# Kernel tuning notes

Hardware: AMD Instinct MI355X
Metric: run time of the kernel (lower is better)

Reference implementation:

```python
import jax, jax.numpy as jnp
import numpy as np

N, LQ, DM = 8, 2500, 256
NH, NL, NP, NZ = 8, 4, 8, 4
DH = DM // NH
SPATIAL = np.array([[64, 176], [32, 88], [16, 44], [8, 22]], dtype=np.int32)
LEN_IN = int((SPATIAL[:, 0] * SPATIAL[:, 1]).sum())


def setup_inputs() -> dict:
    key = jax.random.key(0)
    ks = jax.random.split(key, 10)
    query = jax.random.normal(ks[0], (N, LQ, DM), dtype=jnp.float32)
    query_pos = jax.random.normal(ks[1], (N, LQ, DM), dtype=jnp.float32)
    reference_points = jax.random.uniform(ks[2], (N, LQ, NZ, 2), dtype=jnp.float32)
    input_flatten = jax.random.normal(ks[3], (N, LEN_IN, DM), dtype=jnp.float32)
    input_spatial_shapes = jnp.asarray(SPATIAL)
    lsi = np.concatenate([[0], np.cumsum(SPATIAL[:, 0] * SPATIAL[:, 1])[:-1]]).astype(np.int32)
    input_level_start_index = jnp.asarray(lsi)
    # learned params (Linear: y = x @ W + b, W is (in, out))
    Wv = jax.random.normal(ks[4], (DM, DM), dtype=jnp.float32) * (1.0 / np.sqrt(DM))
    bv = jnp.zeros((DM,), dtype=jnp.float32)
    Wo = jax.random.normal(ks[5], (DM, NH * NL * NP * 2), dtype=jnp.float32) * 0.02
    bo = jax.random.normal(ks[6], (NH * NL * NP * 2,), dtype=jnp.float32) * 1.0
    Wa = jax.random.normal(ks[7], (DM, NH * NL * NP), dtype=jnp.float32) * 0.02
    ba = jnp.zeros((NH * NL * NP,), dtype=jnp.float32)
    return {"query": query, "query_pos": query_pos, "reference_points": reference_points,
            "input_flatten": input_flatten, "input_spatial_shapes": input_spatial_shapes,
            "input_level_start_index": input_level_start_index,
            "Wv": Wv, "bv": bv, "Wo": Wo, "bo": bo, "Wa": Wa, "ba": ba}


def _sample_level(v, h, w, loc):
    """Bilinear sample (grid_sample, align_corners=False, zero padding).
    v:   (N, h*w, NH, DH) level feature map
    loc: (N, Lq, NH, P, 2) normalized locations in [0,1] (x, y)
    returns (N, NH, Lq, P, DH)
    """
    n, hw, nh, dh = v.shape
    lq, p = loc.shape[1], loc.shape[3]
    x = loc[..., 0] * w - 0.5
    y = loc[..., 1] * h - 0.5
    x0f = jnp.floor(x)
    y0f = jnp.floor(y)
    wx = x - x0f
    wy = y - y0f
    x0 = x0f.astype(jnp.int32)
    y0 = y0f.astype(jnp.int32)
    vt = v.transpose(0, 2, 1, 3).reshape(n * nh, hw, dh)

    def gather(xi, yi, wgt):
        valid = ((xi >= 0) & (xi < w) & (yi >= 0) & (yi < h)).astype(v.dtype)
        idx = jnp.clip(yi, 0, h - 1) * w + jnp.clip(xi, 0, w - 1)  # (N,Lq,NH,P)
        idx = idx.transpose(0, 2, 1, 3).reshape(n * nh, lq * p)
        g = jnp.take_along_axis(vt, idx[:, :, None], axis=1)  # (N*NH, Lq*P, DH)
        wv = (wgt * valid).transpose(0, 2, 1, 3).reshape(n * nh, lq * p)
        return g * wv[:, :, None]

    out = (gather(x0, y0, (1 - wx) * (1 - wy))
           + gather(x0 + 1, y0, wx * (1 - wy))
           + gather(x0, y0 + 1, (1 - wx) * wy)
           + gather(x0 + 1, y0 + 1, wx * wy))
    return out.reshape(n, nh, lq, p, dh)


def _forward(query, query_pos, reference_points, input_flatten, spatial, Wv, bv, Wo, bo, Wa, ba):
    n, lq, _ = query.shape
    len_in = input_flatten.shape[1]
    # projections
    value = (input_flatten @ Wv + bv).reshape(n, len_in, NH, DH)
    off = (query @ Wo + bo).reshape(n, lq, NH, NL, NP, 2)
    aw = jax.nn.softmax((query @ Wa + ba).reshape(n, lq, NH, NL * NP), axis=-1)
    aw = aw.reshape(n, lq, NH, NL, NP)
    # normalize offsets by (W_l, H_l), add to Z-anchor reference points
    norm = jnp.asarray(np.stack([spatial[:, 1], spatial[:, 0]], -1), dtype=query.dtype)  # (NL,2)
    off = off / norm[None, None, None, :, None, :]
    off = off.reshape(n, lq, NH, NL, NP // NZ, NZ, 2)
    ref = reference_points[:, :, None, None, None, :, :]  # (N,Lq,1,1,1,NZ,2)
    loc = (ref + off).reshape(n, lq, NH, NL, NP, 2)
    # multi-scale deformable sampling + weighted reduction
    out = jnp.zeros((n, lq, NH, DH), dtype=query.dtype)
    start = 0
    for lvl in range(NL):
        h, w = int(spatial[lvl, 0]), int(spatial[lvl, 1])
        v_l = value[:, start:start + h * w]
        start += h * w
        samp = _sample_level(v_l, h, w, loc[:, :, :, lvl])  # (N,NH,Lq,NP,DH)
        out = out + jnp.einsum('nhqpd,nqhp->nqhd', samp, aw[:, :, :, lvl])
    return out.reshape(n, lq, DM)


def reference(query, query_pos, reference_points, input_flatten, input_spatial_shapes,
              input_level_start_index, Wv, bv, Wo, bo, Wa, ba):
    spatial = np.asarray(jax.device_get(input_spatial_shapes))
    return _forward(query, query_pos, reference_points, input_flatten, spatial,
                    Wv, bv, Wo, bo, Wa, ba)
```

## Files before the change

kernel.cpp:

```cpp
#include <hip/hip_runtime.h>
#include <hip/hip_fp16.h>

#define N_BATCH 8
#define LQ_     2500
#define DM_     256
#define NH_     8
#define NL_     4
#define NP_     8
#define DH_     32
#define LEN_IN_ 14960
#define KDIM    256

#define MV_   119680
#define MQ_   20000
#define NBMV  935
#define NBMQ  157
#define NVB   1872
#define NCB   960

__constant__ int c_w[4]     = {176, 88, 44, 22};
__constant__ int c_h[4]     = {64, 32, 16, 8};
__constant__ int c_start[4] = {0, 11264, 14080, 14784};

using bf16x8 = __attribute__((ext_vector_type(8))) short;
using f32x4  = __attribute__((ext_vector_type(4))) float;

#define GLDS16(g, l)                                                         \
    __builtin_amdgcn_global_load_lds(                                        \
        (const __attribute__((address_space(1))) void*)(g),                  \
        (__attribute__((address_space(3))) void*)(l), 16, 0, 0)

static __device__ inline float fdot2_u(unsigned int p, unsigned int w, float c) {
    float r;
    asm("v_dot2_f32_f16 %0, %1, %2, %3" : "=v"(r) : "v"(p), "v"(w), "v"(c));
    return r;
}

static __device__ inline void split_bf16(float v, unsigned short& hi, unsigned short& lo) {
    unsigned int u = __float_as_uint(v);
    hi = (unsigned short)(u >> 16);
    float hif = __uint_as_float(u & 0xFFFF0000u);
    float l = v - hif;
    lo = (unsigned short)(__float_as_uint(l) >> 16);
}

static __device__ inline unsigned short f2bf_rne(float v) {
    unsigned int u = __float_as_uint(v);
    u += 0x7FFFu + ((u >> 16) & 1u);
    return (unsigned short)(u >> 16);
}

static __device__ inline unsigned short f2h_rne(float v) {
    _Float16 h = (_Float16)v;
    return __builtin_bit_cast(unsigned short, h);
}

__global__ __launch_bounds__(256) void conv_weights(
    const float* __restrict__ Wv, const float* __restrict__ Wo,
    const float* __restrict__ Wa, const float* __restrict__ bo,
    const float* __restrict__ ba,
    unsigned short* __restrict__ Wv_hi, unsigned short* __restrict__ Wv_lo,
    unsigned short* __restrict__ Wc_hi, unsigned short* __restrict__ Wc_lo,
    float* __restrict__ bcomb)
{
    int id = blockIdx.x * 256 + threadIdx.x;
    if (id < 256 * 256) {
        int n = id >> 8, k = id & 255;
        unsigned short h, l;
        split_bf16(Wv[k * 256 + n], h, l);
        Wv_hi[id] = h; Wv_lo[id] = l;
    } else {
        int id2 = id - 65536;
        if (id2 < 768 * 256) {
            int n = id2 >> 8, k = id2 & 255;
            float v = (n < 512) ? Wo[k * 512 + n] : Wa[k * 256 + (n - 512)];
            unsigned short h, l;
            split_bf16(v, h, l);
            Wc_hi[id2] = h; Wc_lo[id2] = l;
        }
    }
    if (id < 768) bcomb[id] = (id < 512) ? bo[id] : ba[id - 512];
}

__global__ __launch_bounds__(512, 4) void gemm2(
    const float* __restrict__ Av,
    const float* __restrict__ Aq,
    const unsigned short* __restrict__ Wvh, const unsigned short* __restrict__ Wvl,
    const unsigned short* __restrict__ Wch, const unsigned short* __restrict__ Wcl,
    const float* __restrict__ bv, const float* __restrict__ bc,
    float* __restrict__ Cq,
    unsigned short* __restrict__ Cv)
{
    __shared__ __align__(16) unsigned short As [4096];
    __shared__ __align__(16) unsigned short Bhs[4096];
    __shared__ __align__(16) unsigned short Bls[4096];

    const int tid = threadIdx.x;
    const int bid = blockIdx.x;
    const bool is_comb = (bid >= NVB);

    const float* A;
    const unsigned short *Bth, *Btl;
    const float* bias;
    int by, bx, M, N;
    if (is_comb) {
        int cid = bid - NVB;
        int xcd = cid & 7, j = cid >> 3;
        by = xcd + 8 * (j / 6); bx = j % 6;
        if (by >= NBMQ) return;
        A = Aq; Bth = Wch; Btl = Wcl; bias = bc;
        M = MQ_; N = 768;
    } else {
        int xcd = bid & 7, j = bid >> 3;
        by = xcd + 8 * (j >> 1); bx = j & 1;
        if (by >= NBMV) return;
        A = Av; Bth = Wvh; Btl = Wvl; bias = bv;
        M = MV_; N = 256;
    }

    const int row0 = by << 7, col0 = bx << 7;
    const int lane = tid & 63, wave = tid >> 6;
    const int wrow = (wave & 1) << 6, wcol = (wave >> 1) << 5;
    const int r16  = lane & 15, quad = lane >> 4;

    const int srow = tid >> 2, skq = tid & 3;
    const int arow = min(row0 + srow, M - 1);
    const float* gA = A + (size_t)arow * KDIM + skq * 8;
    const unsigned short* gBh = Bth + (size_t)(col0 + srow) * KDIM + skq * 8;
    const unsigned short* gBl = Btl + (size_t)(col0 + srow) * KDIM + skq * 8;
    unsigned short* lBh = &Bhs[wave << 9];
    unsigned short* lBl = &Bls[wave << 9];
    const int aoff = srow * 32 + skq * 8;

    float4 pa[2][2];
#pragma unroll
    for (int s = 0; s < 2; ++s) {
        pa[s][0] = *(const float4*)(gA + s * 32);
        pa[s][1] = *(const float4*)(gA + s * 32 + 4);
    }

    f32x4 acc[4][2];
#pragma unroll
    for (int i = 0; i < 4; ++i)
#pragma unroll
        for (int j = 0; j < 2; ++j) acc[i][j] = (f32x4){0.f, 0.f, 0.f, 0.f};

#pragma unroll
    for (int kt = 0; kt < 8; ++kt) {
        const int cur = kt & 1;

        GLDS16(gBh + kt * 32, lBh);
        GLDS16(gBl + kt * 32, lBl);
        {
            bf16x8 hv;
            hv[0] = (short)f2bf_rne(pa[cur][0].x); hv[1] = (short)f2bf_rne(pa[cur][0].y);
            hv[2] = (short)f2bf_rne(pa[cur][0].z); hv[3] = (short)f2bf_rne(pa[cur][0].w);
            hv[4] = (short)f2bf_rne(pa[cur][1].x); hv[5] = (short)f2bf_rne(pa[cur][1].y);
            hv[6] = (short)f2bf_rne(pa[cur][1].z); hv[7] = (short)f2bf_rne(pa[cur][1].w);
            *(bf16x8*)&As[aoff] = hv;
        }
        __syncthreads();

        if (kt < 6) {
            pa[cur][0] = *(const float4*)(gA + (kt + 2) * 32);
            pa[cur][1] = *(const float4*)(gA + (kt + 2) * 32 + 4);
        }

        bf16x8 fbh[2], fbl[2], fa[4];
#pragma unroll
        for (int tn = 0; tn < 2; ++tn) {
            int n = wcol + tn * 16 + r16;
            fbh[tn] = *(const bf16x8*)&Bhs[n * 32 + (quad << 3)];
            fbl[tn] = *(const bf16x8*)&Bls[n * 32 + (quad << 3)];
        }
#pragma unroll
        for (int tm = 0; tm < 4; ++tm)
            fa[tm] = *(const bf16x8*)&As[(wrow + tm * 16 + r16) * 32 + (quad << 3)];
#pragma unroll
        for (int tm = 0; tm < 4; ++tm)
#pragma unroll
            for (int tn = 0; tn < 2; ++tn) {
                acc[tm][tn] = __builtin_amdgcn_mfma_f32_16x16x32_bf16(fa[tm], fbl[tn], acc[tm][tn], 0, 0, 0);
                acc[tm][tn] = __builtin_amdgcn_mfma_f32_16x16x32_bf16(fa[tm], fbh[tn], acc[tm][tn], 0, 0, 0);
            }
        __syncthreads();
    }

    float bvs[2];
#pragma unroll
    for (int tn = 0; tn < 2; ++tn) bvs[tn] = bias[col0 + wcol + tn * 16 + r16];
#pragma unroll
    for (int tm = 0; tm < 4; ++tm) {
#pragma unroll
        for (int i = 0; i < 4; ++i) {
            int row = row0 + wrow + tm * 16 + (quad << 2) + i;
            if (row < M) {
                if (is_comb) {
                    float* crow = Cq + (size_t)row * N + col0 + wcol + r16;
#pragma unroll
                    for (int tn = 0; tn < 2; ++tn)
                        crow[tn * 16] = acc[tm][tn][i] + bvs[tn];
                } else {
                    int n   = row / LEN_IN_;
                    int pix = row - n * LEN_IN_;
#pragma unroll
                    for (int tn = 0; tn < 2; ++tn) {
                        int col = col0 + wcol + tn * 16 + r16;
                        int h = col >> 5, dh = col & 31;
                        size_t addr = ((size_t)(n * NH_ + h) * LEN_IN_ + pix) * DH_ + dh;
                        Cv[addr] = f2h_rne(acc[tm][tn][i] + bvs[tn]);
                    }
                }
            }
        }
    }
}

__global__ __launch_bounds__(256, 4) void ms_sample(
    const unsigned short* __restrict__ value,
    const float* __restrict__ comb,
    const float* __restrict__ ref_pts,
    float* __restrict__ out)
{
    __shared__ uint4 s_desc[64][33];

    const int b     = blockIdx.x;
    const int xcd   = b & 7;
    const int j     = b >> 3;
    const int slice = (j / 40) * 8 + xcd;
    const int chunk = j % 40;
    const int n     = slice >> 3, h = slice & 7;
    const int q0    = chunk * 64;
    const int tid   = threadIdx.x;

    {
        int ql = tid >> 2, l = tid & 3;
        int q  = q0 + ql;
        if (q < LQ_) {
            int nq = n * LQ_ + q;
            const float* row = comb + (size_t)nq * 768;

            float4 L0 = *(const float4*)&row[512 + h * 32 + l * 8];
            float4 L1 = *(const float4*)&row[512 + h * 32 + l * 8 + 4];
            float lg[8] = {L0.x, L0.y, L0.z, L0.w, L1.x, L1.y, L1.z, L1.w};
            float m = lg[0];
#pragma unroll
            for (int i = 1; i < 8; ++i) m = fmaxf(m, lg[i]);
            m = fmaxf(m, __shfl_xor(m, 1));
            m = fmaxf(m, __shfl_xor(m, 2));
            float e[8], s = 0.f;
#pragma unroll
            for (int i = 0; i < 8; ++i) { e[i] = __expf(lg[i] - m); s += e[i]; }
            s += __shfl_xor(s, 1);
            s += __shfl_xor(s, 2);
            float inv = 1.f / s;

            float4 R0 = *(const float4*)&ref_pts[(size_t)nq * 8];
            float4 R1 = *(const float4*)&ref_pts[(size_t)nq * 8 + 4];
            float rx[4] = {R0.x, R0.z, R1.x, R1.z};
            float ry[4] = {R0.y, R0.w, R1.y, R1.w};

            float off[16];
#pragma unroll
            for (int i = 0; i < 4; ++i)
                *(float4*)&off[i * 4] = *(const float4*)&row[h * 64 + l * 16 + i * 4];

            float wl = (float)c_w[l], hl = (float)c_h[l];
            int wli = c_w[l], hli = c_h[l], st = c_start[l];
#pragma unroll
            for (int p = 0; p < 8; ++p) {
                int z = p & 3;
                float a = e[p] * inv;
                float x = rx[z] * wl + off[p * 2 + 0] - 0.5f;
                float y = ry[z] * hl + off[p * 2 + 1] - 0.5f;
                float x0f = floorf(x), y0f = floorf(y);
                int   x0 = (int)x0f,  y0 = (int)y0f;
                float wx = x - x0f,   wy = y - y0f;
                unsigned short ix[4];
                float wt[4];
#pragma unroll
                for (int jj = 0; jj < 4; ++jj) {
                    int xi = x0 + (jj & 1);
                    int yi = y0 + (jj >> 1);
                    float w = ((jj & 1) ? wx : 1.f - wx) * ((jj >> 1) ? wy : 1.f - wy);
                    bool valid = (xi >= 0) && (xi < wli) && (yi >= 0) && (yi < hli);
                    int xc = min(max(xi, 0), wli - 1);
                    int yc = min(max(yi, 0), hli - 1);
                    ix[jj] = (unsigned short)(yc * wli + xc);
                    wt[jj] = valid ? a * w : 0.f;
                }
                uint4 d;
                d.x = (unsigned int)(st + ix[0]) | ((unsigned int)(st + ix[1]) << 16);
                d.y = (unsigned int)(st + ix[2]) | ((unsigned int)(st + ix[3]) << 16);
                __half2 h01 = __floats2half2_rn(wt[0], wt[1]);
                __half2 h23 = __floats2half2_rn(wt[2], wt[3]);
                d.z = *(unsigned int*)&h01;
                d.w = *(unsigned int*)&h23;
                s_desc[ql][l * 8 + p] = d;
            }
        }
    }
    __syncthreads();

    int ql = tid >> 2, dhg = tid & 3;
    int q  = q0 + ql;
    if (q >= LQ_) return;
    int nq = n * LQ_ + q;
    const unsigned short* vb = value
        + ((size_t)(n * NH_ + h) * LEN_IN_) * DH_ + dhg * 8;

    float acc[8];
#pragma unroll
    for (int i = 0; i < 8; ++i) acc[i] = 0.f;

#pragma unroll 4
    for (int s = 0; s < 32; ++s) {
        uint4 d = s_desc[ql][s];
        int i0 = d.x & 0xFFFF, i1 = d.x >> 16;
        int i2 = d.y & 0xFFFF, i3 = d.y >> 16;
        uint4 v0 = *(const uint4*)(vb + i0 * DH_);
        uint4 v1 = *(const uint4*)(vb + i1 * DH_);
        uint4 v2 = *(const uint4*)(vb + i2 * DH_);
        uint4 v3 = *(const uint4*)(vb + i3 * DH_);
        acc[0] = fdot2_u(__builtin_amdgcn_perm(v1.x, v0.x, 0x05040100u), d.z, acc[0]);
        acc[1] = fdot2_u(__builtin_amdgcn_perm(v1.x, v0.x, 0x07060302u), d.z, acc[1]);
        acc[2] = fdot2_u(__builtin_amdgcn_perm(v1.y, v0.y, 0x05040100u), d.z, acc[2]);
        acc[3] = fdot2_u(__builtin_amdgcn_perm(v1.y, v0.y, 0x07060302u), d.z, acc[3]);
        acc[4] = fdot2_u(__builtin_amdgcn_perm(v1.z, v0.z, 0x05040100u), d.z, acc[4]);
        acc[5] = fdot2_u(__builtin_amdgcn_perm(v1.z, v0.z, 0x07060302u), d.z, acc[5]);
        acc[6] = fdot2_u(__builtin_amdgcn_perm(v1.w, v0.w, 0x05040100u), d.z, acc[6]);
        acc[7] = fdot2_u(__builtin_amdgcn_perm(v1.w, v0.w, 0x07060302u), d.z, acc[7]);
        acc[0] = fdot2_u(__builtin_amdgcn_perm(v3.x, v2.x, 0x05040100u), d.w, acc[0]);
        acc[1] = fdot2_u(__builtin_amdgcn_perm(v3.x, v2.x, 0x07060302u), d.w, acc[1]);
        acc[2] = fdot2_u(__builtin_amdgcn_perm(v3.y, v2.y, 0x05040100u), d.w, acc[2]);
        acc[3] = fdot2_u(__builtin_amdgcn_perm(v3.y, v2.y, 0x07060302u), d.w, acc[3]);
        acc[4] = fdot2_u(__builtin_amdgcn_perm(v3.z, v2.z, 0x05040100u), d.w, acc[4]);
        acc[5] = fdot2_u(__builtin_amdgcn_perm(v3.z, v2.z, 0x07060302u), d.w, acc[5]);
        acc[6] = fdot2_u(__builtin_amdgcn_perm(v3.w, v2.w, 0x05040100u), d.w, acc[6]);
        acc[7] = fdot2_u(__builtin_amdgcn_perm(v3.w, v2.w, 0x07060302u), d.w, acc[7]);
    }

    float* op = out + (size_t)nq * 256 + h * 32 + dhg * 8;
    *(float4*)&op[0] = make_float4(acc[0], acc[1], acc[2], acc[3]);
    *(float4*)&op[4] = make_float4(acc[4], acc[5], acc[6], acc[7]);
}

extern "C" void kernel_launch(void* const* d_in, const int* in_sizes, int n_in,
                              void* d_out, int out_size, void* d_ws, size_t ws_size,
                              hipStream_t stream)
{
    const float* query         = (const float*)d_in[0];
    const float* ref_pts       = (const float*)d_in[2];
    const float* input_flatten = (const float*)d_in[3];
    const float* Wv            = (const float*)d_in[6];
    const float* bv            = (const float*)d_in[7];
    const float* Wo            = (const float*)d_in[8];
    const float* bo            = (const float*)d_in[9];
    const float* Wa            = (const float*)d_in[10];
    const float* ba            = (const float*)d_in[11];
    float* out = (float*)d_out;

    char* ws = (char*)d_ws;
    size_t o = 0;
    unsigned short* Wv_hi = (unsigned short*)(ws + o); o += 256 * 256 * 2;
    unsigned short* Wv_lo = (unsigned short*)(ws + o); o += 256 * 256 * 2;
    unsigned short* Wc_hi = (unsigned short*)(ws + o); o += 768 * 256 * 2;
    unsigned short* Wc_lo = (unsigned short*)(ws + o); o += 768 * 256 * 2;
    float*          bcomb = (float*)(ws + o);          o += 768 * 4;
    o = (o + 511) & ~(size_t)511;
    unsigned short* value = (unsigned short*)(ws + o); o += (size_t)119680 * 256 * 2;
    o = (o + 511) & ~(size_t)511;
    float* combq = (float*)(ws + o); o += (size_t)20000 * 768 * 4;

    hipLaunchKernelGGL(conv_weights, dim3(1024), dim3(256), 0, stream,
                       Wv, Wo, Wa, bo, ba, Wv_hi, Wv_lo, Wc_hi, Wc_lo, bcomb);
    hipLaunchKernelGGL(gemm2, dim3(NVB + NCB), dim3(512), 0, stream,
                       input_flatten, query, Wv_hi, Wv_lo, Wc_hi, Wc_lo,
                       bv, bcomb, combq, value);
    hipLaunchKernelGGL(ms_sample, dim3(2560), dim3(256), 0, stream,
                       value, combq, ref_pts, out);
}
```

Before: 340.9 us.

## Double-buffer LDS tiles in gemm2 to drop one barrier per K step

```diff
diff --git a/kernel.cpp b/kernel.cpp
--- a/kernel.cpp
+++ b/kernel.cpp
@@ -53,6 +53,15 @@
 static __device__ inline unsigned short f2h_rne(float v) {
     _Float16 h = (_Float16)v;
     return __builtin_bit_cast(unsigned short, h);
+}
+
+static __device__ inline bf16x8 cvt8_rne(float4 a, float4 b) {
+    bf16x8 hv;
+    hv[0] = (short)f2bf_rne(a.x); hv[1] = (short)f2bf_rne(a.y);
+    hv[2] = (short)f2bf_rne(a.z); hv[3] = (short)f2bf_rne(a.w);
+    hv[4] = (short)f2bf_rne(b.x); hv[5] = (short)f2bf_rne(b.y);
+    hv[6] = (short)f2bf_rne(b.z); hv[7] = (short)f2bf_rne(b.w);
+    return hv;
 }
 
 __global__ __launch_bounds__(256) void conv_weights(
@@ -91,9 +100,9 @@
     float* __restrict__ Cq,
     unsigned short* __restrict__ Cv)
 {
-    __shared__ __align__(16) unsigned short As [4096];
-    __shared__ __align__(16) unsigned short Bhs[4096];
-    __shared__ __align__(16) unsigned short Bls[4096];
+    __shared__ __align__(16) unsigned short As [2][4096];
+    __shared__ __align__(16) unsigned short Bhs[2][4096];
+    __shared__ __align__(16) unsigned short Bls[2][4096];
 
     const int tid = threadIdx.x;
     const int bid = blockIdx.x;
@@ -128,16 +137,19 @@
     const float* gA = A + (size_t)arow * KDIM + skq * 8;
     const unsigned short* gBh = Bth + (size_t)(col0 + srow) * KDIM + skq * 8;
     const unsigned short* gBl = Btl + (size_t)(col0 + srow) * KDIM + skq * 8;
-    unsigned short* lBh = &Bhs[wave << 9];
-    unsigned short* lBl = &Bls[wave << 9];
-    const int aoff = srow * 32 + skq * 8;
-
+    const int lbase = wave << 9;
+    const int aoff  = srow * 32 + skq * 8;
+
+    GLDS16(gBh, &Bhs[0][lbase]);
+    GLDS16(gBl, &Bls[0][lbase]);
     float4 pa[2][2];
 #pragma unroll
     for (int s = 0; s < 2; ++s) {
         pa[s][0] = *(const float4*)(gA + s * 32);
         pa[s][1] = *(const float4*)(gA + s * 32 + 4);
     }
+    *(bf16x8*)&As[0][aoff] = cvt8_rne(pa[0][0], pa[0][1]);
+    __syncthreads();
 
     f32x4 acc[4][2];
 #pragma unroll
@@ -147,20 +159,14 @@
 
 #pragma unroll
     for (int kt = 0; kt < 8; ++kt) {
-        const int cur = kt & 1;
-
-        GLDS16(gBh + kt * 32, lBh);
-        GLDS16(gBl + kt * 32, lBl);
-        {
-            bf16x8 hv;
-            hv[0] = (short)f2bf_rne(pa[cur][0].x); hv[1] = (short)f2bf_rne(pa[cur][0].y);
-            hv[2] = (short)f2bf_rne(pa[cur][0].z); hv[3] = (short)f2bf_rne(pa[cur][0].w);
-            hv[4] = (short)f2bf_rne(pa[cur][1].x); hv[5] = (short)f2bf_rne(pa[cur][1].y);
-            hv[6] = (short)f2bf_rne(pa[cur][1].z); hv[7] = (short)f2bf_rne(pa[cur][1].w);
-            *(bf16x8*)&As[aoff] = hv;
-        }
-        __syncthreads();
-
+        const int cur = kt & 1, nxt = cur ^ 1;
+
+        if (kt < 7) {
+            GLDS16(gBh + (kt + 1) * 32, &Bhs[nxt][lbase]);
+            GLDS16(gBl + (kt + 1) * 32, &Bls[nxt][lbase]);
+            *(bf16x8*)&As[nxt][aoff] =
+                cvt8_rne(pa[nxt][0], pa[nxt][1]);
+        }
         if (kt < 6) {
             pa[cur][0] = *(const float4*)(gA + (kt + 2) * 32);
             pa[cur][1] = *(const float4*)(gA + (kt + 2) * 32 + 4);
@@ -170,12 +176,12 @@
 #pragma unroll
         for (int tn = 0; tn < 2; ++tn) {
             int n = wcol + tn * 16 + r16;
-            fbh[tn] = *(const bf16x8*)&Bhs[n * 32 + (quad << 3)];
-            fbl[tn] = *(const bf16x8*)&Bls[n * 32 + (quad << 3)];
+            fbh[tn] = *(const bf16x8*)&Bhs[cur][n * 32 + (quad << 3)];
+            fbl[tn] = *(const bf16x8*)&Bls[cur][n * 32 + (quad << 3)];
         }
 #pragma unroll
         for (int tm = 0; tm < 4; ++tm)
-            fa[tm] = *(const bf16x8*)&As[(wrow + tm * 16 + r16) * 32 + (quad << 3)];
+            fa[tm] = *(const bf16x8*)&As[cur][(wrow + tm * 16 + r16) * 32 + (quad << 3)];
 #pragma unroll
         for (int tm = 0; tm < 4; ++tm)
 #pragma unroll
@@ -183,6 +189,7 @@
                 acc[tm][tn] = __builtin_amdgcn_mfma_f32_16x16x32_bf16(fa[tm], fbl[tn], acc[tm][tn], 0, 0, 0);
                 acc[tm][tn] = __builtin_amdgcn_mfma_f32_16x16x32_bf16(fa[tm], fbh[tn], acc[tm][tn], 0, 0, 0);
             }
+
         __syncthreads();
     }
 
```

New measurement: 333.7 us. 1.02x faster.
